# Kernel optimization log

Measured on AMD Instinct MI355X. Metric: run time of the kernel, lower is better.

## Reference

```python
import jax, jax.numpy as jnp
import numpy as np

NEG_SLOPE = 0.2  # PyG GATv2Conv default negative_slope


def gatv2_layer(x, src, dst, edge_attr, Wl, bl, Wr, br, We, att, bias):
    # Faithful PyG GATv2Conv (heads=H, concat=True, edge_dim=1, add_self_loops=True,
    # fill_value='mean', share_weights=False).
    N = x.shape[0]
    H, C = att.shape
    xl = (x @ Wl + bl).reshape(N, H, C)  # source-side transform (x_j)
    xr = (x @ Wr + br).reshape(N, H, C)  # target-side transform (x_i)
    valid = src != dst  # PyG removes pre-existing self loops before adding its own
    w = valid.astype(x.dtype)[:, None]
    # self-loop edge_attr = per-dst mean of incoming (non-self-loop) edge_attr
    sums = jax.ops.segment_sum(edge_attr * w, dst, num_segments=N)
    cnts = jax.ops.segment_sum(w, dst, num_segments=N)
    loop_attr = jnp.where(cnts > 0, sums / jnp.maximum(cnts, 1.0), 0.0)  # [N,1]
    e = (edge_attr @ We).reshape(-1, H, C)      # lin_edge (bias=False)  [E,H,C]
    e_loop = (loop_attr @ We).reshape(N, H, C)  # [N,H,C]
    # GATv2 scoring: leaky_relu(x_i + x_j + e) . att
    m = jax.nn.leaky_relu(xl[src] + xr[dst] + e, NEG_SLOPE)      # [E,H,C]
    score = jnp.where(valid[:, None], (m * att).sum(-1), -jnp.inf)  # [E,H]
    m_loop = jax.nn.leaky_relu(xl + xr + e_loop, NEG_SLOPE)      # [N,H,C]
    score_loop = (m_loop * att).sum(-1)                          # [N,H]
    # segment softmax over incoming edges + self loop, per dst node
    smax = jnp.maximum(jax.ops.segment_max(score, dst, num_segments=N), score_loop)
    ex = jnp.where(valid[:, None], jnp.exp(score - smax[dst]), 0.0)
    ex_loop = jnp.exp(score_loop - smax)
    denom = jax.ops.segment_sum(ex, dst, num_segments=N) + ex_loop  # [N,H]
    alpha = ex / denom[dst]
    alpha_loop = ex_loop / denom
    # aggregate alpha * x_j (transformed source features)
    out = jax.ops.segment_sum(alpha[..., None] * xl[src], dst, num_segments=N)
    out = out + alpha_loop[..., None] * xl
    return out.reshape(N, H * C) + bias


def setup_inputs() -> dict:
    key = jax.random.key(0)
    ks = jax.random.split(key, 16)
    N, E, D_IN, HID, H, D_OUT = 20000, 640000, 128, 32, 4, 64
    HC = H * HID  # 128
    s = lambda fan_in: 1.0 / np.sqrt(fan_in)
    inp = {
        "x": jax.random.normal(ks[0], (N, D_IN), jnp.float32),
        "edge_index": jax.random.randint(ks[1], (2, E), 0, N, jnp.int64),
        "edge_attr": jax.random.normal(ks[2], (E, 1), jnp.float32),
        "Wl1": jax.random.normal(ks[3], (D_IN, HC), jnp.float32) * s(D_IN),
        "bl1": jnp.zeros((HC,), jnp.float32),
        "Wr1": jax.random.normal(ks[4], (D_IN, HC), jnp.float32) * s(D_IN),
        "br1": jnp.zeros((HC,), jnp.float32),
        "We1": jax.random.normal(ks[5], (1, HC), jnp.float32),
        "att1": jax.random.normal(ks[6], (H, HID), jnp.float32) * s(HID),
        "b1": jnp.zeros((HC,), jnp.float32),
        "Wl2": jax.random.normal(ks[7], (HC, HC), jnp.float32) * s(HC),
        "bl2": jnp.zeros((HC,), jnp.float32),
        "Wr2": jax.random.normal(ks[8], (HC, HC), jnp.float32) * s(HC),
        "br2": jnp.zeros((HC,), jnp.float32),
        "We2": jax.random.normal(ks[9], (1, HC), jnp.float32),
        "att2": jax.random.normal(ks[10], (H, HID), jnp.float32) * s(HID),
        "b2": jnp.zeros((HC,), jnp.float32),
        "Wo": jax.random.normal(ks[11], (HC, D_OUT), jnp.float32) * s(HC),
        "bo": jnp.zeros((D_OUT,), jnp.float32),
    }
    return inp


def reference(x, edge_index, edge_attr, Wl1, bl1, Wr1, br1, We1, att1, b1,
              Wl2, bl2, Wr2, br2, We2, att2, b2, Wo, bo):
    src, dst = edge_index[0], edge_index[1]
    h = jax.nn.elu(gatv2_layer(x, src, dst, edge_attr, Wl1, bl1, Wr1, br1, We1, att1, b1))
    h = jax.nn.elu(gatv2_layer(h, src, dst, edge_attr, Wl2, bl2, Wr2, br2, We2, att2, b2))
    return h @ Wo + bo
```

## Files before the change

### kernel.cpp

```cpp
#include <hip/hip_runtime.h>
#include <math.h>


#define SLOT 96


__global__ void build_kernel(const int* __restrict__ ei, const float* __restrict__ ea,
                             int E, int* __restrict__ deg, int2* __restrict__ csr) {
    int e = blockIdx.x * blockDim.x + threadIdx.x;
    if (e < E) {
        int s = ei[e], d = ei[E + e];
        if (s != d) {
            int pos = atomicAdd(&deg[d], 1);
            if (pos < SLOT)
                csr[d * SLOT + pos] = make_int2(s * 128, __float_as_int(ea[e]));
        }
    }
}


#define FMA_ROW(accrow, aval, bvec)                                            \
    accrow[0] = fmaf(aval, bvec.x, accrow[0]);                                 \
    accrow[1] = fmaf(aval, bvec.y, accrow[1]);                                 \
    accrow[2] = fmaf(aval, bvec.z, accrow[2]);                                 \
    accrow[3] = fmaf(aval, bvec.w, accrow[3]);

__global__ __launch_bounds__(256) void gemm_dual(
    const float* __restrict__ A,
    const float* __restrict__ B0, const float* __restrict__ bias0,
    float* __restrict__ C0,
    const float* __restrict__ B1, const float* __restrict__ bias1,
    float* __restrict__ C1,
    int M, int NCOL) {
    __shared__ float As[64 * 64];
    __shared__ float Bs[2][64 * 64];
    const int tid = threadIdx.x;
    const int tx = tid & 15, ty = tid >> 4;
    const int row0 = blockIdx.x * 64;
    const int col0 = blockIdx.y * 64;
    const int bcol = 4 * tx;
    const int arow = 4 * ty;

    float acc[2][4][4];
#pragma unroll
    for (int mi = 0; mi < 2; ++mi)
#pragma unroll
        for (int r = 0; r < 4; ++r)
            acc[mi][r][0] = acc[mi][r][1] = acc[mi][r][2] = acc[mi][r][3] = 0.f;

#pragma unroll
    for (int kh = 0; kh < 128; kh += 64) {
        __syncthreads();
#pragma unroll
        for (int it = 0; it < 4; ++it) {
            int i = tid * 4 + it * 1024;
            int r = i >> 6, k = i & 63;
            int gr = row0 + r;
            float4 v = make_float4(0.f, 0.f, 0.f, 0.f);
            if (gr < M) v = *(const float4*)&A[(size_t)gr * 128 + kh + k];
            *(float4*)&As[r * 64 + k] = v;
        }
#pragma unroll
        for (int it = 0; it < 4; ++it) {
            int i = tid * 4 + it * 1024;
            int k = i >> 6, cc = i & 63;
            *(float4*)&Bs[0][k * 64 + cc] =
                *(const float4*)&B0[(size_t)(kh + k) * NCOL + col0 + cc];
            *(float4*)&Bs[1][k * 64 + cc] =
                *(const float4*)&B1[(size_t)(kh + k) * NCOL + col0 + cc];
        }
        __syncthreads();

#pragma unroll 2
        for (int kk = 0; kk < 64; kk += 4) {
            float4 a0 = *(const float4*)&As[(arow + 0) * 64 + kk];
            float4 a1 = *(const float4*)&As[(arow + 1) * 64 + kk];
            float4 a2 = *(const float4*)&As[(arow + 2) * 64 + kk];
            float4 a3 = *(const float4*)&As[(arow + 3) * 64 + kk];
#pragma unroll
            for (int mi = 0; mi < 2; ++mi) {
                float4 b0 = *(const float4*)&Bs[mi][(kk + 0) * 64 + bcol];
                float4 b1 = *(const float4*)&Bs[mi][(kk + 1) * 64 + bcol];
                float4 b2 = *(const float4*)&Bs[mi][(kk + 2) * 64 + bcol];
                float4 b3 = *(const float4*)&Bs[mi][(kk + 3) * 64 + bcol];
                FMA_ROW(acc[mi][0], a0.x, b0) FMA_ROW(acc[mi][1], a1.x, b0)
                FMA_ROW(acc[mi][2], a2.x, b0) FMA_ROW(acc[mi][3], a3.x, b0)
                FMA_ROW(acc[mi][0], a0.y, b1) FMA_ROW(acc[mi][1], a1.y, b1)
                FMA_ROW(acc[mi][2], a2.y, b1) FMA_ROW(acc[mi][3], a3.y, b1)
                FMA_ROW(acc[mi][0], a0.z, b2) FMA_ROW(acc[mi][1], a1.z, b2)
                FMA_ROW(acc[mi][2], a2.z, b2) FMA_ROW(acc[mi][3], a3.z, b2)
                FMA_ROW(acc[mi][0], a0.w, b3) FMA_ROW(acc[mi][1], a1.w, b3)
                FMA_ROW(acc[mi][2], a2.w, b3) FMA_ROW(acc[mi][3], a3.w, b3)
            }
        }
    }

#pragma unroll
    for (int mi = 0; mi < 2; ++mi) {
        const float* bias = mi ? bias1 : bias0;
        float* C = mi ? C1 : C0;
        float4 bv = *(const float4*)&bias[col0 + bcol];
#pragma unroll
        for (int rr = 0; rr < 4; ++rr) {
            int gr = row0 + arow + rr;
            if (gr < M) {
                float4 o = make_float4(acc[mi][rr][0] + bv.x, acc[mi][rr][1] + bv.y,
                                       acc[mi][rr][2] + bv.z, acc[mi][rr][3] + bv.w);
                *(float4*)&C[(size_t)gr * NCOL + col0 + bcol] = o;
            }
        }
    }
}


#define GAT_M2 51.9370199f
#define LOG2E 1.44269504f

template <int ROR>
__device__ __forceinline__ float dpp_ror_add(float x) {
    int y = __builtin_amdgcn_update_dpp(0, __float_as_int(x), 0x120 + ROR, 0xf, 0xf, true);
    return x + __int_as_float(y);
}

__device__ __forceinline__ void gat_update(float xlx, float xly, float a,
                                           float xrx, float xry,
                                           float wex, float wey,
                                           float atx, float aty,
                                           float& den,
                                           float& acc0, float& acc1) {
    float t0 = fmaf(a, wex, xlx + xrx);
    float t1 = fmaf(a, wey, xly + xry);
    t0 = fmaxf(t0, 0.2f * t0);
    t1 = fmaxf(t1, 0.2f * t1);
    float sc = fmaf(t0, atx, t1 * aty);
    sc = dpp_ror_add<1>(sc);
    sc = dpp_ror_add<2>(sc);
    sc = dpp_ror_add<4>(sc);
    sc = dpp_ror_add<8>(sc);
    float pw = exp2f(sc - GAT_M2);
    den += pw;
    acc0 = fmaf(pw, xlx, acc0);
    acc1 = fmaf(pw, xly, acc1);
}

#define GB 16

template <bool FINAL>
__global__ __launch_bounds__(256, 4) void gat_fused(
    const float* __restrict__ xl, const float* __restrict__ xr,
    const int2* __restrict__ csr, const int* __restrict__ deg,
    const float* __restrict__ We, const float* __restrict__ att,
    const float* __restrict__ bias,
    const float* __restrict__ Wo, const float* __restrict__ bo,
    float* __restrict__ out, int N) {
    __shared__ float hb[4][128];
    const int node = (blockIdx.x * blockDim.x + threadIdx.x) >> 6;
    const int wid = threadIdx.x >> 6;
    const int lane = threadIdx.x & 63;
    if (node >= N) return;
    const int c = lane * 2;

    const float2 xrv = *(const float2*)&xr[(size_t)node * 128 + c];
    const float2 wev = *(const float2*)&We[c];
    float2 atv = *(const float2*)&att[c];
    atv.x *= LOG2E; atv.y *= LOG2E;

    float den = 0.f, acc0 = 0.f, acc1 = 0.f;
    float easum = 0.f;
    int dg = __builtin_amdgcn_readfirstlane(deg[node]);
    dg = dg < SLOT ? dg : SLOT;
    const int snode = __builtin_amdgcn_readfirstlane(node);
    const int beg = snode * SLOT;
    const int end = beg + dg;

    int p = beg;
    for (; p + GB <= end; p += GB) {
        int2 cv[GB]; float2 xv[GB];
#pragma unroll
        for (int j = 0; j < GB; ++j) cv[j] = csr[p + j];
#pragma unroll
        for (int j = 0; j < GB; ++j)
            xv[j] = *(const float2*)&xl[cv[j].x + c];
#pragma unroll
        for (int j = 0; j < GB; ++j) {
            float a = __int_as_float(cv[j].y);
            easum += a;
            gat_update(xv[j].x, xv[j].y, a, xrv.x, xrv.y, wev.x, wev.y,
                       atv.x, atv.y, den, acc0, acc1);
        }
    }
    if (p < end) {
        int2 cv[GB]; float2 xv[GB];
#pragma unroll
        for (int j = 0; j < GB; ++j) {
            int q = (p + j < end) ? (p + j) : (end - 1);
            cv[j] = csr[q];
        }
#pragma unroll
        for (int j = 0; j < GB; ++j)
            xv[j] = *(const float2*)&xl[cv[j].x + c];
#pragma unroll
        for (int j = 0; j < GB; ++j)
            if (p + j < end) {
                float a = __int_as_float(cv[j].y);
                easum += a;
                gat_update(xv[j].x, xv[j].y, a, xrv.x, xrv.y, wev.x, wev.y,
                           atv.x, atv.y, den, acc0, acc1);
            }
    }

    const float al = (dg > 0) ? easum / (float)dg : 0.f;
    const float2 xself = *(const float2*)&xl[(size_t)node * 128 + c];
    gat_update(xself.x, xself.y, al, xrv.x, xrv.y, wev.x, wev.y,
               atv.x, atv.y, den, acc0, acc1);

    const float inv = 1.f / den;
    float o0 = acc0 * inv + bias[c];
    float o1 = acc1 * inv + bias[c + 1];
    o0 = o0 > 0.f ? o0 : __expf(o0) - 1.f;
    o1 = o1 > 0.f ? o1 : __expf(o1) - 1.f;

    if (!FINAL) {
        *(float2*)&out[(size_t)node * 128 + c] = make_float2(o0, o1);
    } else {
        hb[wid][c] = o0;
        hb[wid][c + 1] = o1;
        float accv = bo[lane];
#pragma unroll 8
        for (int k = 0; k < 128; ++k)
            accv = fmaf(hb[wid][k], Wo[k * 64 + lane], accv);
        out[(size_t)node * 64 + lane] = accv;
    }
}


extern "C" void kernel_launch(void* const* d_in, const int* in_sizes, int n_in,
                              void* d_out, int out_size, void* d_ws, size_t ws_size,
                              hipStream_t stream) {
    const float* x    = (const float*)d_in[0];
    const int*   ei   = (const int*)d_in[1];
    const float* ea   = (const float*)d_in[2];
    const float* Wl1  = (const float*)d_in[3];
    const float* bl1  = (const float*)d_in[4];
    const float* Wr1  = (const float*)d_in[5];
    const float* br1  = (const float*)d_in[6];
    const float* We1  = (const float*)d_in[7];
    const float* att1 = (const float*)d_in[8];
    const float* b1   = (const float*)d_in[9];
    const float* Wl2  = (const float*)d_in[10];
    const float* bl2  = (const float*)d_in[11];
    const float* Wr2  = (const float*)d_in[12];
    const float* br2  = (const float*)d_in[13];
    const float* We2  = (const float*)d_in[14];
    const float* att2 = (const float*)d_in[15];
    const float* b2   = (const float*)d_in[16];
    const float* Wo   = (const float*)d_in[17];
    const float* bo   = (const float*)d_in[18];
    float* out = (float*)d_out;

    const int N = in_sizes[0] / 128;
    const int E = in_sizes[1] / 2;

    char* base = (char*)d_ws;
    size_t off = 0;
    auto alloc = [&](size_t bytes) -> void* {
        void* p = base + off;
        off += (bytes + 255) & ~(size_t)255;
        return p;
    };
    float* xl  = (float*)alloc((size_t)N * 128 * 4);
    float* xr  = (float*)alloc((size_t)N * 128 * 4);
    float* h   = (float*)alloc((size_t)N * 128 * 4);
    int*   deg = (int*)alloc((size_t)N * 4);
    int2*  csr = (int2*)alloc((size_t)N * SLOT * 8);

    hipMemsetAsync(deg, 0, (size_t)N * 4, stream);
    build_kernel<<<(E + 255) / 256, 256, 0, stream>>>(ei, ea, E, deg, csr);

    const dim3 g2((unsigned)(N + 63) / 64, 2);
    const int fblk = (N + 3) / 4;

    gemm_dual<<<g2, 256, 0, stream>>>(x, Wl1, bl1, xl, Wr1, br1, xr, N, 128);
    gat_fused<false><<<fblk, 256, 0, stream>>>(xl, xr, csr, deg, We1, att1, b1,
                                               nullptr, nullptr, h, N);

    gemm_dual<<<g2, 256, 0, stream>>>(h, Wl2, bl2, xl, Wr2, br2, xr, N, 128);
    gat_fused<true><<<fblk, 256, 0, stream>>>(xl, xr, csr, deg, We2, att2, b2,
                                              Wo, bo, out, N);
}
```

Before: 278.7 us.

## Pad degree counters, prefetch GEMM tiles to registers, raise GAT occupancy

The per-node degree counters are padded to one per 64-byte line so that atomics on neighbouring destinations stop contending for the same cache line. The dual GEMM now issues all global loads for both K halves into registers up front and only then stages them through shared memory, which removes a barrier and overlaps load latency. The launch-bounds occupancy hint on the fused GAT kernel rises from 4 to 6, which risks register spills. Padding makes the counter array and its memset 16 times larger, and the degree reads in the GAT kernel become strided.

```diff
diff --git a/kernel.cpp b/kernel.cpp
--- a/kernel.cpp
+++ b/kernel.cpp
@@ -11,7 +11,7 @@
     if (e < E) {
         int s = ei[e], d = ei[E + e];
         if (s != d) {
-            int pos = atomicAdd(&deg[d], 1);
+            int pos = atomicAdd(&deg[d << 4], 1);
             if (pos < SLOT)
                 csr[d * SLOT + pos] = make_int2(s * 128, __float_as_int(ea[e]));
         }
@@ -41,16 +41,10 @@
     const int bcol = 4 * tx;
     const int arow = 4 * ty;
 
-    float acc[2][4][4];
-#pragma unroll
-    for (int mi = 0; mi < 2; ++mi)
-#pragma unroll
-        for (int r = 0; r < 4; ++r)
-            acc[mi][r][0] = acc[mi][r][1] = acc[mi][r][2] = acc[mi][r][3] = 0.f;
-
-#pragma unroll
-    for (int kh = 0; kh < 128; kh += 64) {
-        __syncthreads();
+    float4 pa[2][4], pb[2][2][4];
+#pragma unroll
+    for (int h = 0; h < 2; ++h) {
+        const int kh = h * 64;
 #pragma unroll
         for (int it = 0; it < 4; ++it) {
             int i = tid * 4 + it * 1024;
@@ -58,16 +52,39 @@
             int gr = row0 + r;
             float4 v = make_float4(0.f, 0.f, 0.f, 0.f);
             if (gr < M) v = *(const float4*)&A[(size_t)gr * 128 + kh + k];
-            *(float4*)&As[r * 64 + k] = v;
+            pa[h][it] = v;
         }
 #pragma unroll
         for (int it = 0; it < 4; ++it) {
             int i = tid * 4 + it * 1024;
             int k = i >> 6, cc = i & 63;
-            *(float4*)&Bs[0][k * 64 + cc] =
-                *(const float4*)&B0[(size_t)(kh + k) * NCOL + col0 + cc];
-            *(float4*)&Bs[1][k * 64 + cc] =
-                *(const float4*)&B1[(size_t)(kh + k) * NCOL + col0 + cc];
+            pb[h][0][it] = *(const float4*)&B0[(size_t)(kh + k) * NCOL + col0 + cc];
+            pb[h][1][it] = *(const float4*)&B1[(size_t)(kh + k) * NCOL + col0 + cc];
+        }
+    }
+
+    float acc[2][4][4];
+#pragma unroll
+    for (int mi = 0; mi < 2; ++mi)
+#pragma unroll
+        for (int r = 0; r < 4; ++r)
+            acc[mi][r][0] = acc[mi][r][1] = acc[mi][r][2] = acc[mi][r][3] = 0.f;
+
+#pragma unroll
+    for (int h = 0; h < 2; ++h) {
+        if (h) __syncthreads();
+#pragma unroll
+        for (int it = 0; it < 4; ++it) {
+            int i = tid * 4 + it * 1024;
+            int r = i >> 6, k = i & 63;
+            *(float4*)&As[r * 64 + k] = pa[h][it];
+        }
+#pragma unroll
+        for (int it = 0; it < 4; ++it) {
+            int i = tid * 4 + it * 1024;
+            int k = i >> 6, cc = i & 63;
+            *(float4*)&Bs[0][k * 64 + cc] = pb[h][0][it];
+            *(float4*)&Bs[1][k * 64 + cc] = pb[h][1][it];
         }
         __syncthreads();
 
@@ -146,7 +163,7 @@
 #define GB 16
 
 template <bool FINAL>
-__global__ __launch_bounds__(256, 4) void gat_fused(
+__global__ __launch_bounds__(256, 6) void gat_fused(
     const float* __restrict__ xl, const float* __restrict__ xr,
     const int2* __restrict__ csr, const int* __restrict__ deg,
     const float* __restrict__ We, const float* __restrict__ att,
@@ -167,7 +184,7 @@
 
     float den = 0.f, acc0 = 0.f, acc1 = 0.f;
     float easum = 0.f;
-    int dg = __builtin_amdgcn_readfirstlane(deg[node]);
+    int dg = __builtin_amdgcn_readfirstlane(deg[node << 4]);
     dg = dg < SLOT ? dg : SLOT;
     const int snode = __builtin_amdgcn_readfirstlane(node);
     const int beg = snode * SLOT;
@@ -271,10 +288,10 @@
     float* xl  = (float*)alloc((size_t)N * 128 * 4);
     float* xr  = (float*)alloc((size_t)N * 128 * 4);
     float* h   = (float*)alloc((size_t)N * 128 * 4);
-    int*   deg = (int*)alloc((size_t)N * 4);
+    int*   deg = (int*)alloc((size_t)N * 16 * 4);
     int2*  csr = (int2*)alloc((size_t)N * SLOT * 8);
 
-    hipMemsetAsync(deg, 0, (size_t)N * 4, stream);
+    hipMemsetAsync(deg, 0, (size_t)N * 16 * 4, stream);
     build_kernel<<<(E + 255) / 256, 256, 0, stream>>>(ei, ea, E, deg, csr);
 
     const dim3 g2((unsigned)(N + 63) / 64, 2);
```

New measurement: 292.2 us. 1.05x slower.
